# Kernel tuning notes

Hardware: AMD Instinct MI355X
Metric: run time of the kernel (lower is better)

## Reference

```python
import jax, jax.numpy as jnp
import numpy as np

N_NODES = 50000
N_EDGES = 800000
IN_CH = 128
HIDDEN = 16
OUT_CH = 64


def setup_inputs() -> dict:
    key = jax.random.key(0)
    ks = jax.random.split(key, 8)
    x = jax.random.normal(ks[0], (N_NODES, IN_CH), dtype=jnp.float32)
    edge_index = jax.random.randint(ks[1], (2, N_EDGES), 0, N_NODES, dtype=jnp.int64)
    s1 = 1.0 / np.sqrt(IN_CH)
    s2 = 1.0 / np.sqrt(HIDDEN)
    W1l = jax.random.uniform(ks[2], (IN_CH, HIDDEN), jnp.float32, -s1, s1)
    b1l = jnp.zeros((HIDDEN,), jnp.float32)
    W1r = jax.random.uniform(ks[3], (IN_CH, HIDDEN), jnp.float32, -s1, s1)
    W2l = jax.random.uniform(ks[4], (HIDDEN, OUT_CH), jnp.float32, -s2, s2)
    b2l = jnp.zeros((OUT_CH,), jnp.float32)
    W2r = jax.random.uniform(ks[5], (HIDDEN, OUT_CH), jnp.float32, -s2, s2)
    return {"x": x, "W1l": W1l, "b1l": b1l, "W1r": W1r,
            "W2l": W2l, "b2l": b2l, "W2r": W2r, "edge_index": edge_index}


def _sage_conv(x, edge_index, Wl, bl, Wr):
    # PyG SAGEConv (mean aggr): out = lin_l(mean_j x_j) + lin_r(x_i)
    src, dst = edge_index[0], edge_index[1]
    msg_sum = jax.ops.segment_sum(x[src], dst, num_segments=N_NODES)  # [N, d]
    deg = jax.ops.segment_sum(jnp.ones((edge_index.shape[1],), x.dtype), dst,
                              num_segments=N_NODES)
    mean = msg_sum / jnp.maximum(deg, 1.0)[:, None]
    return mean @ Wl + bl + x @ Wr


def reference(x, W1l, b1l, W1r, W2l, b2l, W2r, edge_index):
    h = _sage_conv(x, edge_index, W1l, b1l, W1r)
    h = jax.nn.relu(h)
    # dropout p=0.5 is identity in eval mode (training=False)
    out = _sage_conv(h, edge_index, W2l, b2l, W2r)
    return jax.nn.log_softmax(out, axis=1)
```

## Files before the change

kernel.cpp:

```cpp
#include <hip/hip_runtime.h>
#include <stdint.h>

#define N_NODES 50000
#define N_EDGES 800000
#define IN_CH 128
#define HIDDEN 16
#define OUT_CH 64
#define ROWCAP 48
#define NBB 782
#define NPAD (NBB * 64)
#define OVFCAP 64

#define PEB 1024
#define PB ((N_EDGES + PEB - 1) / PEB)
#define LB ((N_NODES + 31) / 32)

__global__ __launch_bounds__(256) void k_front(
    const int* __restrict__ ei,
    int* __restrict__ bucket,
    uint16_t* __restrict__ base16,
    const float* __restrict__ x,
    const float* __restrict__ W1l, const float* __restrict__ W1r,
    float* __restrict__ y1, float* __restrict__ z1)
{
    __shared__ float sW[IN_CH][36];
    __shared__ float sx[32][IN_CH + 1];
    const int t = threadIdx.x;

    if (blockIdx.x < PB) {
        int* stg  = (int*)&sW[0][0];
        int* hist = (int*)&sx[0][0];
        int* cur  = hist + 784;
        int* wsum = cur + 784;
        int* lflag = wsum + 4;
        const int blk = blockIdx.x;
        const int e0 = blk * PEB;
        const int lane = t & 63;
        const int wid  = t >> 6;

        if (t < 64) {
            const int v = ei[2 * t + 1];
            const unsigned long long b = __ballot(v != 0);
            if (t == 0) *lflag = (b == 0ull);
        }
        for (int i = t; i < 784; i += 256) hist[i] = 0;
        __syncthreads();
        const int is64 = *lflag;

        int srcs[4], dsts[4];
        #pragma unroll
        for (int k = 0; k < 4; ++k) {
            const int e = e0 + t + k * 256;
            int src = 0, dst = -1;
            if (e < N_EDGES) {
                if (is64) {
                    src = ((const int2*)ei)[e].x;
                    dst = ((const int2*)ei)[N_EDGES + e].x;
                } else {
                    src = ei[e];
                    dst = ei[N_EDGES + e];
                }
                atomicAdd(&hist[dst >> 6], 1);
            }
            srcs[k] = src; dsts[k] = dst;
        }
        __syncthreads();

        int tot = 0;
        #pragma unroll
        for (int j = 0; j < 4; ++j) {
            const int idx = 4 * t + j;
            if (idx < 784) tot += hist[idx];
        }
        int inc = tot;
        #pragma unroll
        for (int off = 1; off < 64; off <<= 1) {
            const int u = __shfl_up(inc, off);
            if (lane >= off) inc += u;
        }
        if (lane == 63) wsum[wid] = inc;
        __syncthreads();
        if (t == 0) {
            int run = 0;
            #pragma unroll
            for (int w = 0; w < 4; ++w) { const int v = wsum[w]; wsum[w] = run; run += v; }
        }
        __syncthreads();
        int run = inc - tot + wsum[wid];
        #pragma unroll
        for (int j = 0; j < 4; ++j) {
            const int idx = 4 * t + j;
            if (idx < 784) {
                cur[idx] = run;
                base16[blk * 784 + idx] = (uint16_t)run;
                run += hist[idx];
            }
        }
        __syncthreads();

        #pragma unroll
        for (int k = 0; k < 4; ++k) {
            if (dsts[k] >= 0) {
                const int bin = dsts[k] >> 6;
                const int pos = atomicAdd(&cur[bin], 1);
                stg[pos] = ((dsts[k] & 63) << 16) | srcs[k];
            }
        }
        __syncthreads();

        ((int4*)(bucket + (size_t)blk * PEB))[t] = ((const int4*)stg)[t];
        return;
    }

    for (int i = t; i < IN_CH * HIDDEN; i += 256) {
        int k = i / HIDDEN, c = i % HIDDEN;
        sW[k][c]      = W1l[i];
        sW[k][c + 16] = W1r[i];
    }

    const int node0 = (blockIdx.x - PB) * 32;
    for (int i = t; i < 32 * (IN_CH / 4); i += 256) {
        int r    = i / (IN_CH / 4);
        int col4 = i % (IN_CH / 4);
        int node = node0 + r;
        float4 v = make_float4(0.f, 0.f, 0.f, 0.f);
        if (node < N_NODES)
            v = ((const float4*)x)[node * (IN_CH / 4) + col4];
        sx[r][col4 * 4 + 0] = v.x;
        sx[r][col4 * 4 + 1] = v.y;
        sx[r][col4 * 4 + 2] = v.z;
        sx[r][col4 * 4 + 3] = v.w;
    }
    __syncthreads();

    const int r    = t & 31;
    const int og   = t >> 5;
    const int node = node0 + r;

    float4 acc = make_float4(0.f, 0.f, 0.f, 0.f);
    #pragma unroll 4
    for (int k = 0; k < IN_CH; ++k) {
        const float xv = sx[r][k];
        const float4 w4 = *(const float4*)&sW[k][og * 4];
        acc.x += xv * w4.x;
        acc.y += xv * w4.y;
        acc.z += xv * w4.z;
        acc.w += xv * w4.w;
    }

    if (node < N_NODES) {
        const int oc = og * 4;
        float vals[4] = {acc.x, acc.y, acc.z, acc.w};
        #pragma unroll
        for (int j = 0; j < 4; ++j) {
            int o = oc + j;
            if (o < HIDDEN) y1[node * HIDDEN + o]            = vals[j];
            else            z1[node * HIDDEN + (o - HIDDEN)] = vals[j];
        }
    }
}

__global__ __launch_bounds__(256) void k_bin_h(
    const int* __restrict__ bucket, const uint16_t* __restrict__ base16,
    uint16_t* __restrict__ row, int* __restrict__ cnt,
    int* __restrict__ govf, int* __restrict__ ovfcnt,
    const float* __restrict__ y1, float* __restrict__ z1h,
    const float* __restrict__ b1l)
{
    __shared__ __align__(16) uint16_t stg[64][ROWCAP];
    __shared__ int cntl[64];
    __shared__ int ovfc;
    __shared__ int govf_l[OVFCAP];
    const int t = threadIdx.x;
    const int b = blockIdx.x;

    if (t < 64) cntl[t] = 0;
    if (t == 64) ovfc = 0;
    __syncthreads();

    for (int pb = t; pb < PB; pb += 256) {
        const int lo = base16[pb * 784 + b];
        const int hi = base16[pb * 784 + b + 1];
        const int* bp = bucket + (size_t)pb * PEB;
        for (int i = lo; i < hi; ++i) {
            const int w   = bp[i];
            const int nl  = (w >> 16) & 63;
            const int src = w & 0xFFFF;
            const int pos = atomicAdd(&cntl[nl], 1);
            if (pos < ROWCAP) {
                stg[nl][pos] = (uint16_t)src;
            } else {
                const int o = atomicAdd(&ovfc, 1);
                if (o < OVFCAP) { govf[b * OVFCAP + o] = w; govf_l[o] = w; }
            }
        }
    }
    __syncthreads();

    {
        const uint4* s4 = (const uint4*)stg;
        uint4* d4 = (uint4*)(row + (size_t)b * 64 * ROWCAP);
        for (int i = t; i < 384; i += 256) d4[i] = s4[i];
        if (t < 64) cnt[b * 64 + t] = cntl[t];
        if (t == 64) ovfcnt[b] = min(ovfc, OVFCAP);
    }

    const int nl = t >> 2;
    const int q  = t & 3;
    const int n  = b * 64 + nl;
    const int dgr   = cntl[nl];
    const int slots = dgr < ROWCAP ? dgr : ROWCAP;

    float4 s = make_float4(0.f, 0.f, 0.f, 0.f);
    int i = 0;
    for (; i + 4 <= slots; i += 4) {
        const int j0 = stg[nl][i + 0];
        const int j1 = stg[nl][i + 1];
        const int j2 = stg[nl][i + 2];
        const int j3 = stg[nl][i + 3];
        const float4 v0 = ((const float4*)(y1 + j0 * HIDDEN))[q];
        const float4 v1 = ((const float4*)(y1 + j1 * HIDDEN))[q];
        const float4 v2 = ((const float4*)(y1 + j2 * HIDDEN))[q];
        const float4 v3 = ((const float4*)(y1 + j3 * HIDDEN))[q];
        s.x += (v0.x + v1.x) + (v2.x + v3.x);
        s.y += (v0.y + v1.y) + (v2.y + v3.y);
        s.z += (v0.z + v1.z) + (v2.z + v3.z);
        s.w += (v0.w + v1.w) + (v2.w + v3.w);
    }
    for (; i < slots; ++i) {
        const int j = stg[nl][i];
        const float4 v = ((const float4*)(y1 + j * HIDDEN))[q];
        s.x += v.x; s.y += v.y; s.z += v.z; s.w += v.w;
    }

    if (dgr > ROWCAP) {
        const int on = min(ovfc, OVFCAP);
        for (int o = 0; o < on; ++o) {
            const int w = govf_l[o];
            if (((w >> 16) & 63) == nl) {
                const float4 v = ((const float4*)(y1 + (w & 0xFFFF) * HIDDEN))[q];
                s.x += v.x; s.y += v.y; s.z += v.z; s.w += v.w;
            }
        }
    }

    if (n < N_NODES) {
        const float inv = 1.0f / fmaxf((float)dgr, 1.0f);
        const float4 b4 = ((const float4*)b1l)[q];
        float4* zp = (float4*)(z1h + (size_t)n * HIDDEN) + q;
        const float4 z4 = *zp;
        float4 hv;
        hv.x = fmaxf(s.x * inv + b4.x + z4.x, 0.f);
        hv.y = fmaxf(s.y * inv + b4.y + z4.y, 0.f);
        hv.z = fmaxf(s.z * inv + b4.z + z4.z, 0.f);
        hv.w = fmaxf(s.w * inv + b4.w + z4.w, 0.f);
        *zp = hv;
    }
}

__device__ __forceinline__ float4 gather_rows_f4(
    const float* __restrict__ feat, const uint16_t* __restrict__ rp,
    int slots, int ri, int q)
{
    float4 s = make_float4(0.f, 0.f, 0.f, 0.f);
    int i = 0;
    while (i + 16 < slots) {
        const int j0 = rp[i + ri];
        const int idx1 = i + 16 + ri;
        const bool p1 = idx1 < slots;
        const int j1 = p1 ? rp[idx1] : 0;
        const float4 v0 = ((const float4*)(feat + j0 * HIDDEN))[q];
        float4 v1 = make_float4(0.f, 0.f, 0.f, 0.f);
        if (p1) v1 = ((const float4*)(feat + j1 * HIDDEN))[q];
        s.x += v0.x + v1.x; s.y += v0.y + v1.y;
        s.z += v0.z + v1.z; s.w += v0.w + v1.w;
        i += 32;
    }
    if (i + ri < slots) {
        const int j = rp[i + ri];
        const float4 v = ((const float4*)(feat + j * HIDDEN))[q];
        s.x += v.x; s.y += v.y; s.z += v.z; s.w += v.w;
    }
    #pragma unroll
    for (int off = 4; off <= 32; off <<= 1) {
        s.x += __shfl_xor(s.x, off);
        s.y += __shfl_xor(s.y, off);
        s.z += __shfl_xor(s.z, off);
        s.w += __shfl_xor(s.w, off);
    }
    return s;
}

__global__ __launch_bounds__(1024) void k_out(
    const int* __restrict__ cnt, const uint16_t* __restrict__ row,
    const int* __restrict__ govf, const int* __restrict__ ovfcnt,
    const float* __restrict__ h,
    const float* __restrict__ W2l, const float* __restrict__ b2l,
    const float* __restrict__ W2r,
    float* __restrict__ out)
{
    __shared__ float sW[HIDDEN][2][OUT_CH];
    __shared__ float sm[16][HIDDEN];
    __shared__ float sh[16][HIDDEN];
    const int t = threadIdx.x;

    const int lane = t & 63;
    const int wid  = t >> 6;
    const int n = blockIdx.x * 16 + wid;
    const int q  = lane & 3;
    const int ri = lane >> 2;

    const int dgr   = cnt[n];
    const int slots = dgr < ROWCAP ? dgr : ROWCAP;
    const uint16_t* rp = row + (size_t)n * ROWCAP;

    float4 s = gather_rows_f4(h, rp, slots, ri, q);

    if (dgr > ROWCAP) {
        const int b = n >> 6;
        const int on = ovfcnt[b];
        for (int o = 0; o < on; ++o) {
            const int w = govf[b * OVFCAP + o];
            if (((w >> 16) & 63) == (n & 63)) {
                const float4 v = ((const float4*)(h + (w & 0xFFFF) * HIDDEN))[q];
                s.x += v.x; s.y += v.y; s.z += v.z; s.w += v.w;
            }
        }
    }

    if (lane < 4) {
        const float inv = 1.0f / fmaxf((float)dgr, 1.0f);
        float4 m4;
        m4.x = s.x * inv; m4.y = s.y * inv; m4.z = s.z * inv; m4.w = s.w * inv;
        ((float4*)&sm[wid][0])[q] = m4;
        ((float4*)&sh[wid][0])[q] = ((const float4*)(h + (size_t)n * HIDDEN))[q];
    }

    {
        const int k = t / OUT_CH, c2 = t % OUT_CH;
        sW[k][0][c2] = W2l[t];
        sW[k][1][c2] = W2r[t];
    }
    __syncthreads();

    float acc = b2l[lane];
    #pragma unroll
    for (int k = 0; k < HIDDEN; ++k)
        acc += sm[wid][k] * sW[k][0][lane] + sh[wid][k] * sW[k][1][lane];

    float mx = acc;
    #pragma unroll
    for (int off = 32; off > 0; off >>= 1)
        mx = fmaxf(mx, __shfl_xor(mx, off));
    float ex = expf(acc - mx);
    float sum = ex;
    #pragma unroll
    for (int off = 32; off > 0; off >>= 1)
        sum += __shfl_xor(sum, off);

    out[(size_t)n * OUT_CH + lane] = acc - mx - logf(sum);
}

extern "C" void kernel_launch(void* const* d_in, const int* in_sizes, int n_in,
                              void* d_out, int out_size, void* d_ws, size_t ws_size,
                              hipStream_t stream)
{
    const float* x   = (const float*)d_in[0];
    const float* W1l = (const float*)d_in[1];
    const float* b1l = (const float*)d_in[2];
    const float* W1r = (const float*)d_in[3];
    const float* W2l = (const float*)d_in[4];
    const float* b2l = (const float*)d_in[5];
    const float* W2r = (const float*)d_in[6];
    const int*   ei  = (const int*)d_in[7];
    float* out = (float*)d_out;

    const size_t NH = (size_t)N_NODES * HIDDEN;
    int*   bucket = (int*)d_ws;
    float* bufA   = (float*)(bucket + (size_t)PB * PEB);
    float* bufB   = bufA + NH;
    int*   cnt    = (int*)(bufB + NH);
    int*   govf   = cnt + NPAD;
    int*   ovfcnt = govf + NBB * OVFCAP;
    uint16_t* base16 = (uint16_t*)(ovfcnt + NBB + 2);
    uint16_t* row    = base16 + (size_t)PB * 784;

    k_front<<<PB + LB, 256, 0, stream>>>(ei, bucket, base16,
                                         x, W1l, W1r, bufA, bufB);

    k_bin_h<<<NBB, 256, 0, stream>>>(bucket, base16, row, cnt, govf, ovfcnt,
                                     bufA, bufB, b1l);

    k_out<<<N_NODES / 16, 1024, 0, stream>>>(cnt, row, govf, ovfcnt, bufB,
                                             W2l, b2l, W2r, out);
}
```

Before: 78.62 us.

## Fuse three stages into one persistent cooperative kernel with grid syncs

Merges the partition/linear, bin-and-hidden, and output stages into a single cooperative kernel. Each block loops over the work items of each stage, and the stages are separated by grid-wide syncs instead of separate kernel launches. The goal is to remove launch gaps and tail effects between kernels. In exchange, occupancy is capped by the single shared-memory footprint of the combined kernel, and the output stage drops from 1024-thread blocks to 256-thread work items. If the cooperative launch fails, the code falls back to three separate kernels.

```diff
diff --git a/kernel.cpp b/kernel.cpp
--- a/kernel.cpp
+++ b/kernel.cpp
@@ -1,5 +1,8 @@
 #include <hip/hip_runtime.h>
+#include <hip/hip_cooperative_groups.h>
 #include <stdint.h>
+
+namespace cg = cooperative_groups;
 
 #define N_NODES 50000
 #define N_EDGES 800000
@@ -14,103 +17,106 @@
 #define PEB 1024
 #define PB ((N_EDGES + PEB - 1) / PEB)
 #define LB ((N_NODES + 31) / 32)
-
-__global__ __launch_bounds__(256) void k_front(
-    const int* __restrict__ ei,
-    int* __restrict__ bucket,
-    uint16_t* __restrict__ base16,
-    const float* __restrict__ x,
+#define OB (N_NODES / 4)
+
+#define SMEM_FLOATS (IN_CH * 36 + 32 * (IN_CH + 1))
+
+
+__device__ __forceinline__ void part_body(
+    int blk, float* __restrict__ smem, const int* __restrict__ ei,
+    int* __restrict__ bucket, uint16_t* __restrict__ base16)
+{
+    int* stg   = (int*)smem;
+    int* hist  = stg + 1024;
+    int* cur   = hist + 784;
+    int* wsum  = cur + 784;
+    int* lflag = wsum + 4;
+    const int t = threadIdx.x;
+    const int e0 = blk * PEB;
+    const int lane = t & 63;
+    const int wid  = t >> 6;
+
+    if (t < 64) {
+        const int v = ei[2 * t + 1];
+        const unsigned long long b = __ballot(v != 0);
+        if (t == 0) *lflag = (b == 0ull);
+    }
+    for (int i = t; i < 784; i += 256) hist[i] = 0;
+    __syncthreads();
+    const int is64 = *lflag;
+
+    int srcs[4], dsts[4];
+    #pragma unroll
+    for (int k = 0; k < 4; ++k) {
+        const int e = e0 + t + k * 256;
+        int src = 0, dst = -1;
+        if (e < N_EDGES) {
+            if (is64) {
+                src = ((const int2*)ei)[e].x;
+                dst = ((const int2*)ei)[N_EDGES + e].x;
+            } else {
+                src = ei[e];
+                dst = ei[N_EDGES + e];
+            }
+            atomicAdd(&hist[dst >> 6], 1);
+        }
+        srcs[k] = src; dsts[k] = dst;
+    }
+    __syncthreads();
+
+    int tot = 0;
+    #pragma unroll
+    for (int j = 0; j < 4; ++j) {
+        const int idx = 4 * t + j;
+        if (idx < 784) tot += hist[idx];
+    }
+    int inc = tot;
+    #pragma unroll
+    for (int off = 1; off < 64; off <<= 1) {
+        const int u = __shfl_up(inc, off);
+        if (lane >= off) inc += u;
+    }
+    if (lane == 63) wsum[wid] = inc;
+    __syncthreads();
+    if (t == 0) {
+        int run = 0;
+        #pragma unroll
+        for (int w = 0; w < 4; ++w) { const int v = wsum[w]; wsum[w] = run; run += v; }
+    }
+    __syncthreads();
+    int run = inc - tot + wsum[wid];
+    #pragma unroll
+    for (int j = 0; j < 4; ++j) {
+        const int idx = 4 * t + j;
+        if (idx < 784) {
+            cur[idx] = run;
+            base16[blk * 784 + idx] = (uint16_t)run;
+            run += hist[idx];
+        }
+    }
+    __syncthreads();
+
+    #pragma unroll
+    for (int k = 0; k < 4; ++k) {
+        if (dsts[k] >= 0) {
+            const int bin = dsts[k] >> 6;
+            const int pos = atomicAdd(&cur[bin], 1);
+            stg[pos] = ((dsts[k] & 63) << 16) | srcs[k];
+        }
+    }
+    __syncthreads();
+
+    ((int4*)(bucket + (size_t)blk * PEB))[t] = ((const int4*)stg)[t];
+}
+
+__device__ __forceinline__ void lin1_body(
+    int item, float* __restrict__ smem, const float* __restrict__ x,
     const float* __restrict__ W1l, const float* __restrict__ W1r,
     float* __restrict__ y1, float* __restrict__ z1)
 {
-    __shared__ float sW[IN_CH][36];
-    __shared__ float sx[32][IN_CH + 1];
+    float (*sW)[36] = (float(*)[36])smem;
+    float (*sx)[IN_CH + 1] = (float(*)[IN_CH + 1])(smem + IN_CH * 36);
     const int t = threadIdx.x;
-
-    if (blockIdx.x < PB) {
-        int* stg  = (int*)&sW[0][0];
-        int* hist = (int*)&sx[0][0];
-        int* cur  = hist + 784;
-        int* wsum = cur + 784;
-        int* lflag = wsum + 4;
-        const int blk = blockIdx.x;
-        const int e0 = blk * PEB;
-        const int lane = t & 63;
-        const int wid  = t >> 6;
-
-        if (t < 64) {
-            const int v = ei[2 * t + 1];
-            const unsigned long long b = __ballot(v != 0);
-            if (t == 0) *lflag = (b == 0ull);
-        }
-        for (int i = t; i < 784; i += 256) hist[i] = 0;
-        __syncthreads();
-        const int is64 = *lflag;
-
-        int srcs[4], dsts[4];
-        #pragma unroll
-        for (int k = 0; k < 4; ++k) {
-            const int e = e0 + t + k * 256;
-            int src = 0, dst = -1;
-            if (e < N_EDGES) {
-                if (is64) {
-                    src = ((const int2*)ei)[e].x;
-                    dst = ((const int2*)ei)[N_EDGES + e].x;
-                } else {
-                    src = ei[e];
-                    dst = ei[N_EDGES + e];
-                }
-                atomicAdd(&hist[dst >> 6], 1);
-            }
-            srcs[k] = src; dsts[k] = dst;
-        }
-        __syncthreads();
-
-        int tot = 0;
-        #pragma unroll
-        for (int j = 0; j < 4; ++j) {
-            const int idx = 4 * t + j;
-            if (idx < 784) tot += hist[idx];
-        }
-        int inc = tot;
-        #pragma unroll
-        for (int off = 1; off < 64; off <<= 1) {
-            const int u = __shfl_up(inc, off);
-            if (lane >= off) inc += u;
-        }
-        if (lane == 63) wsum[wid] = inc;
-        __syncthreads();
-        if (t == 0) {
-            int run = 0;
-            #pragma unroll
-            for (int w = 0; w < 4; ++w) { const int v = wsum[w]; wsum[w] = run; run += v; }
-        }
-        __syncthreads();
-        int run = inc - tot + wsum[wid];
-        #pragma unroll
-        for (int j = 0; j < 4; ++j) {
-            const int idx = 4 * t + j;
-            if (idx < 784) {
-                cur[idx] = run;
-                base16[blk * 784 + idx] = (uint16_t)run;
-                run += hist[idx];
-            }
-        }
-        __syncthreads();
-
-        #pragma unroll
-        for (int k = 0; k < 4; ++k) {
-            if (dsts[k] >= 0) {
-                const int bin = dsts[k] >> 6;
-                const int pos = atomicAdd(&cur[bin], 1);
-                stg[pos] = ((dsts[k] & 63) << 16) | srcs[k];
-            }
-        }
-        __syncthreads();
-
-        ((int4*)(bucket + (size_t)blk * PEB))[t] = ((const int4*)stg)[t];
-        return;
-    }
 
     for (int i = t; i < IN_CH * HIDDEN; i += 256) {
         int k = i / HIDDEN, c = i % HIDDEN;
@@ -118,7 +124,7 @@
         sW[k][c + 16] = W1r[i];
     }
 
-    const int node0 = (blockIdx.x - PB) * 32;
+    const int node0 = item * 32;
     for (int i = t; i < 32 * (IN_CH / 4); i += 256) {
         int r    = i / (IN_CH / 4);
         int col4 = i % (IN_CH / 4);
@@ -160,22 +166,22 @@
     }
 }
 
-__global__ __launch_bounds__(256) void k_bin_h(
+__device__ __forceinline__ void binh_body(
+    int b, float* __restrict__ smem,
     const int* __restrict__ bucket, const uint16_t* __restrict__ base16,
     uint16_t* __restrict__ row, int* __restrict__ cnt,
     int* __restrict__ govf, int* __restrict__ ovfcnt,
     const float* __restrict__ y1, float* __restrict__ z1h,
     const float* __restrict__ b1l)
 {
-    __shared__ __align__(16) uint16_t stg[64][ROWCAP];
-    __shared__ int cntl[64];
-    __shared__ int ovfc;
-    __shared__ int govf_l[OVFCAP];
+    uint16_t (*stg)[ROWCAP] = (uint16_t(*)[ROWCAP])smem;
+    int* cntl   = (int*)(smem + 1536);
+    int* ovfc   = cntl + 64;
+    int* govf_l = ovfc + 1;
     const int t = threadIdx.x;
-    const int b = blockIdx.x;
 
     if (t < 64) cntl[t] = 0;
-    if (t == 64) ovfc = 0;
+    if (t == 64) *ovfc = 0;
     __syncthreads();
 
     for (int pb = t; pb < PB; pb += 256) {
@@ -190,7 +196,7 @@
             if (pos < ROWCAP) {
                 stg[nl][pos] = (uint16_t)src;
             } else {
-                const int o = atomicAdd(&ovfc, 1);
+                const int o = atomicAdd(ovfc, 1);
                 if (o < OVFCAP) { govf[b * OVFCAP + o] = w; govf_l[o] = w; }
             }
         }
@@ -198,11 +204,11 @@
     __syncthreads();
 
     {
-        const uint4* s4 = (const uint4*)stg;
+        const uint4* s4 = (const uint4*)&stg[0][0];
         uint4* d4 = (uint4*)(row + (size_t)b * 64 * ROWCAP);
         for (int i = t; i < 384; i += 256) d4[i] = s4[i];
         if (t < 64) cnt[b * 64 + t] = cntl[t];
-        if (t == 64) ovfcnt[b] = min(ovfc, OVFCAP);
+        if (t == 64) ovfcnt[b] = min(*ovfc, OVFCAP);
     }
 
     const int nl = t >> 2;
@@ -234,7 +240,7 @@
     }
 
     if (dgr > ROWCAP) {
-        const int on = min(ovfc, OVFCAP);
+        const int on = min(*ovfc, OVFCAP);
         for (int o = 0; o < on; ++o) {
             const int w = govf_l[o];
             if (((w >> 16) & 63) == nl) {
@@ -256,6 +262,7 @@
         hv.w = fmaxf(s.w * inv + b4.w + z4.w, 0.f);
         *zp = hv;
     }
+    __syncthreads();
 }
 
 __device__ __forceinline__ float4 gather_rows_f4(
@@ -291,22 +298,32 @@
     return s;
 }
 
-__global__ __launch_bounds__(1024) void k_out(
+__device__ __forceinline__ void out_stageW(
+    float* __restrict__ smem,
+    const float* __restrict__ W2l, const float* __restrict__ W2r)
+{
+    const int t = threadIdx.x;
+    for (int i = t; i < HIDDEN * OUT_CH; i += 256) {
+        const int k = i / OUT_CH, c = i % OUT_CH;
+        smem[(k * 2 + 0) * 64 + c] = W2l[i];
+        smem[(k * 2 + 1) * 64 + c] = W2r[i];
+    }
+}
+
+__device__ __forceinline__ void out_body(
+    int item, float* __restrict__ smem,
     const int* __restrict__ cnt, const uint16_t* __restrict__ row,
     const int* __restrict__ govf, const int* __restrict__ ovfcnt,
-    const float* __restrict__ h,
-    const float* __restrict__ W2l, const float* __restrict__ b2l,
-    const float* __restrict__ W2r,
+    const float* __restrict__ h, const float* __restrict__ b2l,
     float* __restrict__ out)
 {
-    __shared__ float sW[HIDDEN][2][OUT_CH];
-    __shared__ float sm[16][HIDDEN];
-    __shared__ float sh[16][HIDDEN];
+    float* sW2 = smem;
+    float* sm  = smem + 2048;
+    float* sh  = smem + 2112;
     const int t = threadIdx.x;
-
     const int lane = t & 63;
     const int wid  = t >> 6;
-    const int n = blockIdx.x * 16 + wid;
+    const int n = item * 4 + wid;
     const int q  = lane & 3;
     const int ri = lane >> 2;
 
@@ -332,21 +349,15 @@
         const float inv = 1.0f / fmaxf((float)dgr, 1.0f);
         float4 m4;
         m4.x = s.x * inv; m4.y = s.y * inv; m4.z = s.z * inv; m4.w = s.w * inv;
-        ((float4*)&sm[wid][0])[q] = m4;
-        ((float4*)&sh[wid][0])[q] = ((const float4*)(h + (size_t)n * HIDDEN))[q];
-    }
-
-    {
-        const int k = t / OUT_CH, c2 = t % OUT_CH;
-        sW[k][0][c2] = W2l[t];
-        sW[k][1][c2] = W2r[t];
-    }
-    __syncthreads();
+        ((float4*)(sm + wid * 16))[q] = m4;
+        ((float4*)(sh + wid * 16))[q] = ((const float4*)(h + (size_t)n * HIDDEN))[q];
+    }
 
     float acc = b2l[lane];
     #pragma unroll
     for (int k = 0; k < HIDDEN; ++k)
-        acc += sm[wid][k] * sW[k][0][lane] + sh[wid][k] * sW[k][1][lane];
+        acc += sm[wid * 16 + k] * sW2[(k * 2) * 64 + lane]
+             + sh[wid * 16 + k] * sW2[(k * 2 + 1) * 64 + lane];
 
     float mx = acc;
     #pragma unroll
@@ -359,6 +370,79 @@
         sum += __shfl_xor(sum, off);
 
     out[(size_t)n * OUT_CH + lane] = acc - mx - logf(sum);
+}
+
+__global__ __launch_bounds__(256) void k_mega(
+    const int* __restrict__ ei, int* __restrict__ bucket,
+    uint16_t* __restrict__ base16,
+    const float* __restrict__ x,
+    const float* __restrict__ W1l, const float* __restrict__ W1r,
+    float* __restrict__ y1, float* __restrict__ z1h,
+    const float* __restrict__ b1l,
+    uint16_t* __restrict__ row, int* __restrict__ cnt,
+    int* __restrict__ govf, int* __restrict__ ovfcnt,
+    const float* __restrict__ W2l, const float* __restrict__ b2l,
+    const float* __restrict__ W2r,
+    float* __restrict__ out)
+{
+    __shared__ __align__(16) float smem[SMEM_FLOATS];
+    cg::grid_group grid = cg::this_grid();
+    const int nb = gridDim.x;
+
+    for (int it = blockIdx.x; it < PB + LB; it += nb) {
+        if (it < PB) part_body(it, smem, ei, bucket, base16);
+        else         lin1_body(it - PB, smem, x, W1l, W1r, y1, z1h);
+        __syncthreads();
+    }
+    grid.sync();
+
+    for (int it = blockIdx.x; it < NBB; it += nb)
+        binh_body(it, smem, bucket, base16, row, cnt, govf, ovfcnt,
+                  y1, z1h, b1l);
+    grid.sync();
+
+    out_stageW(smem, W2l, W2r);
+    __syncthreads();
+    for (int it = blockIdx.x; it < OB; it += nb)
+        out_body(it, smem, cnt, row, govf, ovfcnt, z1h, b2l, out);
+}
+
+__global__ __launch_bounds__(256) void k_front(
+    const int* __restrict__ ei, int* __restrict__ bucket,
+    uint16_t* __restrict__ base16,
+    const float* __restrict__ x,
+    const float* __restrict__ W1l, const float* __restrict__ W1r,
+    float* __restrict__ y1, float* __restrict__ z1)
+{
+    __shared__ __align__(16) float smem[SMEM_FLOATS];
+    if (blockIdx.x < PB) part_body(blockIdx.x, smem, ei, bucket, base16);
+    else                 lin1_body(blockIdx.x - PB, smem, x, W1l, W1r, y1, z1);
+}
+
+__global__ __launch_bounds__(256) void k_bin_h(
+    const int* __restrict__ bucket, const uint16_t* __restrict__ base16,
+    uint16_t* __restrict__ row, int* __restrict__ cnt,
+    int* __restrict__ govf, int* __restrict__ ovfcnt,
+    const float* __restrict__ y1, float* __restrict__ z1h,
+    const float* __restrict__ b1l)
+{
+    __shared__ __align__(16) float smem[SMEM_FLOATS];
+    binh_body(blockIdx.x, smem, bucket, base16, row, cnt, govf, ovfcnt,
+              y1, z1h, b1l);
+}
+
+__global__ __launch_bounds__(256) void k_out(
+    const int* __restrict__ cnt, const uint16_t* __restrict__ row,
+    const int* __restrict__ govf, const int* __restrict__ ovfcnt,
+    const float* __restrict__ h,
+    const float* __restrict__ W2l, const float* __restrict__ b2l,
+    const float* __restrict__ W2r,
+    float* __restrict__ out)
+{
+    __shared__ __align__(16) float smem[SMEM_FLOATS];
+    out_stageW(smem, W2l, W2r);
+    __syncthreads();
+    out_body(blockIdx.x, smem, cnt, row, govf, ovfcnt, h, b2l, out);
 }
 
 extern "C" void kernel_launch(void* const* d_in, const int* in_sizes, int n_in,
@@ -385,12 +469,31 @@
     uint16_t* base16 = (uint16_t*)(ovfcnt + NBB + 2);
     uint16_t* row    = base16 + (size_t)PB * 784;
 
-    k_front<<<PB + LB, 256, 0, stream>>>(ei, bucket, base16,
-                                         x, W1l, W1r, bufA, bufB);
-
-    k_bin_h<<<NBB, 256, 0, stream>>>(bucket, base16, row, cnt, govf, ovfcnt,
-                                     bufA, bufB, b1l);
-
-    k_out<<<N_NODES / 16, 1024, 0, stream>>>(cnt, row, govf, ovfcnt, bufB,
-                                             W2l, b2l, W2r, out);
-}
+    int maxB = 0;
+    hipError_t qe = hipOccupancyMaxActiveBlocksPerMultiprocessor(&maxB, k_mega, 256, 0);
+    int grid = (qe == hipSuccess && maxB > 0) ? maxB * 256 : 0;
+    if (grid > 2048) grid = 2048;
+
+    hipError_t err = hipErrorUnknown;
+    if (grid > 0) {
+        void* args[] = {
+            (void*)&ei, (void*)&bucket, (void*)&base16,
+            (void*)&x, (void*)&W1l, (void*)&W1r,
+            (void*)&bufA, (void*)&bufB, (void*)&b1l,
+            (void*)&row, (void*)&cnt, (void*)&govf, (void*)&ovfcnt,
+            (void*)&W2l, (void*)&b2l, (void*)&W2r, (void*)&out
+        };
+        err = hipLaunchCooperativeKernel(k_mega, dim3(grid), dim3(256),
+                                         args, 0, stream);
+    }
+
+    if (err != hipSuccess) {
+        (void)hipGetLastError();
+        k_front<<<PB + LB, 256, 0, stream>>>(ei, bucket, base16,
+                                             x, W1l, W1r, bufA, bufB);
+        k_bin_h<<<NBB, 256, 0, stream>>>(bucket, base16, row, cnt, govf,
+                                         ovfcnt, bufA, bufB, b1l);
+        k_out<<<OB, 256, 0, stream>>>(cnt, row, govf, ovfcnt, bufB,
+                                      W2l, b2l, W2r, out);
+    }
+}
```

Measured after the change: 257.1 us. 227% more time.
